# Performance work log

Hardware: AMD Instinct MI355X
Metric: run time of the kernel (lower is better)

The kernel has to match this reference:

```python
import jax, jax.numpy as jnp
import numpy as np

S, WD, TD, CE, CH = 512, 300, 100, 20, 20   # seq len, word dim, tag dim, char emb dim, char lstm hidden
H = 512                                      # main LSTM hidden (per direction)
VOC, TVOC, CVOC, LAB, MAXW = 50000, 50, 100, 50, 16


def lstm_scan(x, W_ih, W_hh, b):
    """Unidirectional LSTM over x:[T,D] -> [T,hid]. PyTorch gate order i,f,g,o."""
    hid = W_hh.shape[1]
    def step(carry, xt):
        h, c = carry
        z = xt @ W_ih.T + h @ W_hh.T + b
        i, f, g, o = jnp.split(z, 4)
        c = jax.nn.sigmoid(f) * c + jax.nn.sigmoid(i) * jnp.tanh(g)
        h = jax.nn.sigmoid(o) * jnp.tanh(c)
        return (h, c), h
    h0 = jnp.zeros((hid,), x.dtype)
    _, hs = jax.lax.scan(step, (h0, h0), x)
    return hs


def setup_inputs() -> dict:
    key = jax.random.key(0)
    ks = jax.random.split(key, 40)
    n = lambda i, shape: jax.random.normal(ks[i], shape, jnp.float32) * 0.05
    return {
        "sentence": jax.random.randint(ks[0], (S,), 0, VOC),
        "tags": jax.random.randint(ks[1], (S,), 0, TVOC),
        "chars": jax.random.randint(ks[2], (S, MAXW), 0, CVOC),
        "char_lengths": jnp.maximum(1, jax.random.randint(ks[3], (S,), 0, MAXW + 1)),
        "best_arcs": jax.random.randint(ks[4], (S,), 0, S),
        "word_emb": n(5, (VOC, WD)),
        "tag_emb": n(6, (TVOC, TD)),
        "char_emb": n(7, (CVOC, CE)),
        "att_W": n(8, (1, CE)), "att_b": n(9, (1,)),
        "W_ih_f": n(10, (4 * H, WD + TD)), "W_hh_f": n(11, (4 * H, H)), "b_f": n(12, (4 * H,)),
        "W_ih_b": n(13, (4 * H, WD + TD)), "W_hh_b": n(14, (4 * H, H)), "b_b": n(15, (4 * H,)),
        "cW_ih": n(16, (4 * CH, CE)), "cW_hh": n(17, (4 * CH, CH)), "cb": n(18, (4 * CH,)),
        "arc_dep_W": n(19, (H, 2 * H)), "arc_dep_b": n(20, (H,)),
        "arc_head_W": n(21, (H, 2 * H)), "arc_head_b": n(22, (H,)),
        "label_dep_W": n(23, (H, 2 * H)), "label_dep_b": n(24, (H,)),
        "label_head_W": n(25, (H, 2 * H)), "label_head_b": n(26, (H,)),
        "biaff_arc_W": n(27, (H, H + 1)),
        "biaff_label_W": n(28, (LAB, H + 1, H + 1)),
    }


def reference(sentence, tags, chars, char_lengths, best_arcs,
              word_emb, tag_emb, char_emb, att_W, att_b,
              W_ih_f, W_hh_f, b_f, W_ih_b, W_hh_b, b_b,
              cW_ih, cW_hh, cb,
              arc_dep_W, arc_dep_b, arc_head_W, arc_head_b,
              label_dep_W, label_dep_b, label_head_W, label_head_b,
              biaff_arc_W, biaff_label_W):
    size = sentence.shape[0]
    we = word_emb[sentence]          # [S, WD]
    te = tag_emb[tags]               # [S, TD]

    # --- per-word char LSTM + attention (original python loop, here vmapped over padded words) ---
    ce = char_emb[chars]             # [S, Lmax, CE]
    def per_word(x, L):
        hs = lstm_scan(x, cW_ih, cW_hh, cb)                  # [Lmax, CH]
        hs = hs * (jnp.arange(x.shape[0]) < L)[:, None]      # zero padded steps
        gram = hs.T @ hs                                     # [CH, CH]
        return gram @ att_W.T + att_b                        # [CH, 1]
    char_feats = jax.vmap(per_word)(ce, char_lengths)        # [S, CH, 1]
    char_embeds = char_feats[:, :, 0].T                      # [CH, S] (cat dim=1 in torch)

    # --- main BiLSTM (dropout in eval mode = identity) ---
    embeds = jnp.concatenate([we, te], axis=1)               # [S, WD+TD]
    hf = lstm_scan(embeds, W_ih_f, W_hh_f, b_f)              # [S, H]
    hb = lstm_scan(embeds[::-1], W_ih_b, W_hh_b, b_b)[::-1]  # [S, H]
    lstm_out = jnp.concatenate([hf, hb], axis=1)             # [S, 2H]

    mlp = lambda W, b: jax.nn.relu(lstm_out @ W.T + b)       # MLP(2H -> H)
    arc_dep = mlp(arc_dep_W, arc_dep_b)
    arc_head = mlp(arc_head_W, arc_head_b)
    label_dep = mlp(label_dep_W, label_dep_b)
    label_head = mlp(label_head_W, label_head_b)

    ones = jnp.ones((size, 1), lstm_out.dtype)
    arc_head_a = jnp.concatenate([arc_head, ones], axis=1)     # [S, H+1]
    label_dep_a = jnp.concatenate([label_dep, ones], axis=1)   # [S, H+1]
    label_head_a = jnp.concatenate([label_head, ones], axis=1) # [S, H+1]

    arc_scores = jax.nn.softmax((arc_head_a @ biaff_arc_W.T) @ arc_dep.T, axis=1)  # [S, S]

    # label_head @ W_l @ label_dep^T for every label l -> [LAB, S, S]
    ls = jnp.einsum('sh,lhk,tk->lst', label_head_a, biaff_label_W, label_dep_a)
    sel = ls[:, best_arcs, jnp.arange(size)]                   # [LAB, S]
    label_scores = jax.nn.log_softmax(sel, axis=0)

    return (arc_scores, label_scores, char_embeds)
```

## Files before the change

kernel.cpp:

```cpp
#include <hip/hip_runtime.h>
#include <hip/hip_fp16.h>


static __device__ __forceinline__ float sigm(float x) { return 1.f / (1.f + __expf(-x)); }
static __device__ __forceinline__ float ftanh(float x) {
    x = fminf(15.f, fmaxf(-15.f, x));
    float e = __expf(2.f * x);
    return (e - 1.f) / (e + 1.f);
}

typedef _Float16 h2_t __attribute__((ext_vector_type(2)));
typedef _Float16 h8_t __attribute__((ext_vector_type(8)));
typedef float f4_t __attribute__((ext_vector_type(4)));
union U32H2 { unsigned u; h2_t h; unsigned short s[2]; };

static __device__ __forceinline__ float dot2f(unsigned wa, unsigned hb, float c) {
#if __has_builtin(__builtin_amdgcn_fdot2)
    U32H2 a, b; a.u = wa; b.u = hb;
    return __builtin_amdgcn_fdot2(a.h, b.h, c, false);
#else
    U32H2 a, b; a.u = wa; b.u = hb;
    return c + (float)a.h[0] * (float)b.h[0] + (float)a.h[1] * (float)b.h[1];
#endif
}
static __device__ __forceinline__ unsigned short f2h16(float x) {
    return __half_as_ushort(__float2half(x));
}

__global__ void gather_k(const int* __restrict__ sentence, const int* __restrict__ tags,
                         const float* __restrict__ word_emb, const float* __restrict__ tag_emb,
                         float* __restrict__ embeds) {
    int t = blockIdx.x;
    int w = sentence[t], tg = tags[t];
    for (int j = threadIdx.x; j < 400; j += blockDim.x) {
        float v = (j < 300) ? word_emb[w * 300 + j] : tag_emb[tg * 100 + (j - 300)];
        embeds[t * 400 + j] = v;
    }
}

static __device__ __forceinline__ void gemm_body(
    const float* __restrict__ A, int lda, const float* __restrict__ B, int ldb,
    const float* __restrict__ bias, int bias_stride,
    float* __restrict__ C, int ldc, int M, int K, int revA, int doRelu) {
    __shared__ float As[16][65];
    __shared__ float Bs[16][65];
    int tx = threadIdx.x & 15, ty = threadIdx.x >> 4;
    int bm = blockIdx.y * 64, bn = blockIdx.x * 64;
    float acc[4][4] = {};
    for (int k0 = 0; k0 < K; k0 += 16) {
#pragma unroll
        for (int i = 0; i < 4; ++i) {
            int e = threadIdx.x + i * 256;
            int m = e >> 4, kk = e & 15;
            int row = bm + m; if (revA) row = M - 1 - row;
            As[kk][m] = A[(size_t)row * lda + k0 + kk];
            Bs[kk][m] = B[(size_t)(bn + m) * ldb + k0 + kk];
        }
        __syncthreads();
#pragma unroll
        for (int kk = 0; kk < 16; ++kk) {
            float a0 = As[kk][ty * 4 + 0], a1 = As[kk][ty * 4 + 1];
            float a2 = As[kk][ty * 4 + 2], a3 = As[kk][ty * 4 + 3];
            float b0 = Bs[kk][tx * 4 + 0], b1 = Bs[kk][tx * 4 + 1];
            float b2 = Bs[kk][tx * 4 + 2], b3 = Bs[kk][tx * 4 + 3];
            acc[0][0] += a0 * b0; acc[0][1] += a0 * b1; acc[0][2] += a0 * b2; acc[0][3] += a0 * b3;
            acc[1][0] += a1 * b0; acc[1][1] += a1 * b1; acc[1][2] += a1 * b2; acc[1][3] += a1 * b3;
            acc[2][0] += a2 * b0; acc[2][1] += a2 * b1; acc[2][2] += a2 * b2; acc[2][3] += a2 * b3;
            acc[3][0] += a3 * b0; acc[3][1] += a3 * b1; acc[3][2] += a3 * b2; acc[3][3] += a3 * b3;
        }
        __syncthreads();
    }
#pragma unroll
    for (int i = 0; i < 4; ++i) {
#pragma unroll
        for (int j = 0; j < 4; ++j) {
            int n = bn + tx * 4 + j;
            float v = acc[i][j];
            if (bias) v += bias[(size_t)n * bias_stride];
            if (doRelu) v = fmaxf(v, 0.f);
            C[(size_t)(bm + ty * 4 + i) * ldc + n] = v;
        }
    }
}

__global__ __launch_bounds__(256) void gemm_abT(
    const float* __restrict__ A, int lda, const float* __restrict__ B, int ldb,
    const float* __restrict__ bias, int bias_stride,
    float* __restrict__ C, int ldc, int M, int N, int K, int revA, int doRelu) {
    gemm_body(A, lda, B, ldb, bias, bias_stride, C, ldc, M, K, revA, doRelu);
}

__global__ __launch_bounds__(256) void gemm_heads(
    const float* __restrict__ A,
    const float* W0, const float* B0, float* C0,
    const float* W1, const float* B1, float* C1,
    const float* W2, const float* B2, float* C2,
    const float* W3, const float* B3, float* C3) {
    const float* W; const float* bias; float* C;
    switch (blockIdx.z) {
        case 0: W = W0; bias = B0; C = C0; break;
        case 1: W = W1; bias = B1; C = C1; break;
        case 2: W = W2; bias = B2; C = C2; break;
        default: W = W3; bias = B3; C = C3; break;
    }
    gemm_body(A, 1024, W, 1024, bias, 1, C, 512, 512, 1024, 0, 1);
}

__global__ __launch_bounds__(256) void gemm_xproj(
    const float* __restrict__ A,
    const float* Wf, const float* bf, float* Cf,
    const float* Wb, const float* bb, float* Cb) {
    const float* W = blockIdx.z ? Wb : Wf;
    const float* bias = blockIdx.z ? bb : bf;
    float* C = blockIdx.z ? Cb : Cf;
    gemm_body(A, 400, W, 400, bias, 1, C, 2048, 512, 400, blockIdx.z, 0);
}

__global__ __launch_bounds__(256) void lstm_rec(
    const float* __restrict__ W_hh_f, const float* __restrict__ W_hh_b,
    const float* __restrict__ xpf, const float* __restrict__ xpb,
    float* __restrict__ lstm_out, unsigned long long* hq) {
    int wg = blockIdx.x;
    int dir = wg >> 4, s = wg & 15;
    int tid = threadIdx.x;
    int wv = tid >> 6;
    int lane = tid & 63;
    int g = tid & 31, p = tid >> 5;
    const float* Whh = dir ? W_hh_b : W_hh_f;
    const float* xp = dir ? xpb : xpf;

    __shared__ float red[2][1024];

    unsigned Wreg[4][32];
#pragma unroll
    for (int q = 0; q < 4; ++q) {
        int gr = q * 512 + s * 32 + g;
        const float* wrow = Whh + (size_t)gr * 512 + p * 64;
#pragma unroll
        for (int u = 0; u < 32; ++u) {
            unsigned lo = f2h16(wrow[2 * u]);
            unsigned hi = f2h16(wrow[2 * u + 1]);
            Wreg[q][u] = lo | (hi << 16);
        }
    }

    float c = 0.f;
    unsigned long long* hbase = hq + dir * 512;
    int qidx = wv * 64 + lane;

    for (int t = 0; t < 512; ++t) {
        float x0 = 0.f, x1 = 0.f, x2 = 0.f, x3 = 0.f;
        if (tid < 32) {
            const float* x = xp + (size_t)t * 2048;
            int col = s * 32 + tid;
            x0 = x[col]; x1 = x[512 + col]; x2 = x[1024 + col]; x3 = x[1536 + col];
        }

        unsigned long long* hin = hbase + (t & 1) * 256;
        unsigned tag = (unsigned)t & 0xffffu;
        unsigned long long v = __hip_atomic_load(hin + qidx, __ATOMIC_RELAXED,
                                                 __HIP_MEMORY_SCOPE_AGENT);
        while ((((unsigned)(v >> 16)) & 0xffffu) != tag || ((unsigned)(v >> 48)) != tag)
            v = __hip_atomic_load(hin + qidx, __ATOMIC_RELAXED, __HIP_MEMORY_SCOPE_AGENT);
        unsigned hw = (unsigned)(v & 0xffffu) | (((unsigned)((v >> 32) & 0xffffu)) << 16);

        float a0 = 0.f, a1 = 0.f, a2 = 0.f, a3 = 0.f;
        int half_base = lane & 32;
#pragma unroll
        for (int u = 0; u < 32; ++u) {
            unsigned hwu = (unsigned)__shfl((int)hw, half_base + u);
            a0 = dot2f(Wreg[0][u], hwu, a0);
            a1 = dot2f(Wreg[1][u], hwu, a1);
            a2 = dot2f(Wreg[2][u], hwu, a2);
            a3 = dot2f(Wreg[3][u], hwu, a3);
        }
        float* r = &red[t & 1][p * 128 + g * 4];
        r[0] = a0; r[1] = a1; r[2] = a2; r[3] = a3;
        __syncthreads();

        if (tid < 32) {
            float z0 = 0.f, z1 = 0.f, z2 = 0.f, z3 = 0.f;
            const float* rb = red[t & 1];
#pragma unroll
            for (int pp = 0; pp < 8; ++pp) {
                const float* rr = rb + pp * 128 + tid * 4;
                z0 += rr[0]; z1 += rr[1]; z2 += rr[2]; z3 += rr[3];
            }
            z0 += x0; z1 += x1; z2 += x2; z3 += x3;
            c = sigm(z1) * c + sigm(z0) * ftanh(z2);
            float hn = sigm(z3) * ftanh(c);
            int col = s * 32 + tid;
            int row = dir ? (511 - t) : t;
            lstm_out[(size_t)row * 1024 + dir * 512 + col] = hn;

            unsigned tw = (unsigned)f2h16(hn) | (((unsigned)(t + 1) & 0xffffu) << 16);
            unsigned other = (unsigned)__shfl_down((int)tw, 1);
            if ((tid & 1) == 0) {
                unsigned long long qv = (unsigned long long)tw |
                                        ((unsigned long long)other << 32);
                __hip_atomic_store(hbase + ((t + 1) & 1) * 256 + (col >> 1), qv,
                                   __ATOMIC_RELAXED, __HIP_MEMORY_SCOPE_AGENT);
            }
        }
    }
}

__global__ __launch_bounds__(64) void char_k(
    const int* __restrict__ chars, const int* __restrict__ char_lengths,
    const float* __restrict__ char_emb, const float* __restrict__ att_W,
    const float* __restrict__ att_b, const float* __restrict__ cW_ih,
    const float* __restrict__ cW_hh, const float* __restrict__ cb,
    float* __restrict__ out2) {
    int w = blockIdx.x, tid = threadIdx.x;
    __shared__ float Wih[1600], Whh[1600], cbs[80], attsh[20];
    __shared__ float xsh[20], hsh[20], prodsh[20];
    for (int i = tid; i < 1600; i += 64) { Wih[i] = cW_ih[i]; Whh[i] = cW_hh[i]; }
    for (int i = tid; i < 80; i += 64) cbs[i] = cb[i];
    if (tid < 20) { attsh[tid] = att_W[tid]; hsh[tid] = 0.f; }
    __syncthreads();

    int L = char_lengths[w];
    float c = 0.f, accj = 0.f;
    for (int t = 0; t < 16; ++t) {
        if (tid < 20) xsh[tid] = char_emb[(size_t)chars[w * 16 + t] * 20 + tid];
        __syncthreads();
        float hn = 0.f;
        if (tid < 20) {
            float z[4];
#pragma unroll
            for (int q = 0; q < 4; ++q) {
                int r = q * 20 + tid;
                float sacc = cbs[r];
                for (int d = 0; d < 20; ++d)
                    sacc += Wih[r * 20 + d] * xsh[d] + Whh[r * 20 + d] * hsh[d];
                z[q] = sacc;
            }
            c = sigm(z[1]) * c + sigm(z[0]) * ftanh(z[2]);
            hn = sigm(z[3]) * ftanh(c);
        }
        __syncthreads();
        if (tid < 20) { hsh[tid] = hn; prodsh[tid] = hn * attsh[tid]; }
        __syncthreads();
        if (tid < 20 && t < L) {
            float st = 0.f;
            for (int k = 0; k < 20; ++k) st += prodsh[k];
            accj += hn * st;
        }
        __syncthreads();
    }
    if (tid < 20) out2[tid * 512 + w] = accj + att_b[0];
}

__global__ void uv_k(const int* __restrict__ best_arcs,
                     const float* __restrict__ label_head, const float* __restrict__ label_dep,
                     float* __restrict__ U, float* __restrict__ V) {
    int t = blockIdx.x;
    int ba = best_arcs[t];
    for (int j = threadIdx.x; j < 516; j += blockDim.x) {
        float u = (j < 512) ? label_head[(size_t)ba * 512 + j] : (j == 512 ? 1.f : 0.f);
        float v = (j < 512) ? label_dep[(size_t)t * 512 + j] : (j == 512 ? 1.f : 0.f);
        U[t * 516 + j] = u;
        V[t * 516 + j] = v;
    }
}

__global__ void uconv_k(const float* __restrict__ U, _Float16* __restrict__ Uh) {
    int t = blockIdx.x;
    for (int h = threadIdx.x; h < 544; h += blockDim.x)
        Uh[(size_t)t * 544 + h] = (_Float16)((h < 513) ? U[(size_t)t * 516 + h] : 0.f);
}

__global__ __launch_bounds__(256) void bconv_k(const float* __restrict__ B,
                                               _Float16* __restrict__ Bh) {
    __shared__ _Float16 Ts[64][68];
    int h0 = blockIdx.x * 64, k0 = blockIdx.y * 64, l = blockIdx.z;
    int tid = threadIdx.x;
    const float* Bl = B + (size_t)l * 513 * 513;
    _Float16* BhL = Bh + (size_t)l * 576 * 544;

    int tr = tid >> 4, tc = tid & 15;
#pragma unroll
    for (int i = 0; i < 4; ++i) {
        int hl = tr + i * 16;
        int h = h0 + hl;
#pragma unroll
        for (int j = 0; j < 4; ++j) {
            int k = k0 + tc * 4 + j;
            float v = (h < 513 && k < 513) ? Bl[(size_t)h * 513 + k] : 0.f;
            Ts[hl][tc * 4 + j] = (_Float16)v;
        }
    }
    __syncthreads();

    int cr = tid >> 2;
    int hb = (tid & 3) * 16;
    int hg = h0 + hb;
    if (hg < 544) {
        __align__(16) _Float16 tmp[16];
#pragma unroll
        for (int j = 0; j < 16; ++j) tmp[j] = Ts[hb + j][cr];
        uint4* dst = (uint4*)(BhL + (size_t)(k0 + cr) * 544 + hg);
        dst[0] = ((const uint4*)tmp)[0];
        dst[1] = ((const uint4*)tmp)[1];
    }
}

__global__ __launch_bounds__(256) void label_mfma(
    const _Float16* __restrict__ Uh,
    const _Float16* __restrict__ Bh,
    const float* __restrict__ V,
    float* __restrict__ sel) {
    __shared__ _Float16 Us[64][40];
    __shared__ _Float16 Bs[64][40];
    int l = blockIdx.z;
    int t0 = blockIdx.y * 64, k0 = blockIdx.x * 64;
    int tid = threadIdx.x;
    int w = tid >> 6, lane = tid & 63, m = lane & 15, q = lane >> 4;
    const _Float16* Bl = Bh + (size_t)l * 576 * 544;
    int srow = tid >> 2, scol = (tid & 3) * 8;

    f4_t acc[4];
#pragma unroll
    for (int c = 0; c < 4; ++c) acc[c] = 0;

    for (int h0 = 0; h0 < 544; h0 += 32) {
        uint4 ud = *(const uint4*)(Uh + (size_t)(t0 + srow) * 544 + h0 + scol);
        uint4 bd = *(const uint4*)(Bl + (size_t)(k0 + srow) * 544 + h0 + scol);
        __syncthreads();
        *(uint4*)(&Us[srow][scol]) = ud;
        *(uint4*)(&Bs[srow][scol]) = bd;
        __syncthreads();

        h8_t a  = *(const h8_t*)(&Us[w * 16 + m][q * 8]);
        h8_t b0 = *(const h8_t*)(&Bs[ 0 + m][q * 8]);
        h8_t b1 = *(const h8_t*)(&Bs[16 + m][q * 8]);
        h8_t b2 = *(const h8_t*)(&Bs[32 + m][q * 8]);
        h8_t b3 = *(const h8_t*)(&Bs[48 + m][q * 8]);
        acc[0] = __builtin_amdgcn_mfma_f32_16x16x32_f16(a, b0, acc[0], 0, 0, 0);
        acc[1] = __builtin_amdgcn_mfma_f32_16x16x32_f16(a, b1, acc[1], 0, 0, 0);
        acc[2] = __builtin_amdgcn_mfma_f32_16x16x32_f16(a, b2, acc[2], 0, 0, 0);
        acc[3] = __builtin_amdgcn_mfma_f32_16x16x32_f16(a, b3, acc[3], 0, 0, 0);
    }

    float* selp = sel + (size_t)l * 512;
#pragma unroll
    for (int r = 0; r < 4; ++r) {
        int t = t0 + w * 16 + q * 4 + r;
        float vsum = 0.f;
#pragma unroll
        for (int c = 0; c < 4; ++c) {
            int k = k0 + c * 16 + m;
            float vv = (k < 513) ? V[(size_t)t * 516 + k] : 0.f;
            vsum += acc[c][r] * vv;
        }
#pragma unroll
        for (int off = 1; off < 16; off <<= 1)
            vsum += __shfl_xor(vsum, off);
        if (m == 0) atomicAdd(selp + t, vsum);
    }
}

__global__ __launch_bounds__(256) void label_k(
    const float* __restrict__ U, const float* __restrict__ V,
    const float* __restrict__ BW, float* __restrict__ sel) {
    __shared__ float Us[16][65];
    __shared__ float Bs[16][65];
    __shared__ float selred[64];
    int l = blockIdx.z;
    int t0 = blockIdx.y * 64, k0 = blockIdx.x * 64;
    const float* Bl = BW + (size_t)l * 513 * 513;
    int tx = threadIdx.x & 15, ty = threadIdx.x >> 4;
    float acc[4][4] = {};
    for (int h0 = 0; h0 < 513; h0 += 16) {
#pragma unroll
        for (int i = 0; i < 4; ++i) {
            int e = threadIdx.x + i * 256;
            int a = e >> 4, hh = e & 15;
            int h = h0 + hh;
            Us[hh][a] = (h < 513) ? U[(size_t)(t0 + a) * 516 + h] : 0.f;
            int kc = k0 + a;
            Bs[hh][a] = (h < 513 && kc < 513) ? Bl[(size_t)h * 513 + kc] : 0.f;
        }
        __syncthreads();
#pragma unroll
        for (int hh = 0; hh < 16; ++hh) {
            float a0 = Us[hh][ty * 4 + 0], a1 = Us[hh][ty * 4 + 1];
            float a2 = Us[hh][ty * 4 + 2], a3 = Us[hh][ty * 4 + 3];
            float b0 = Bs[hh][tx * 4 + 0], b1 = Bs[hh][tx * 4 + 1];
            float b2 = Bs[hh][tx * 4 + 2], b3 = Bs[hh][tx * 4 + 3];
            acc[0][0] += a0 * b0; acc[0][1] += a0 * b1; acc[0][2] += a0 * b2; acc[0][3] += a0 * b3;
            acc[1][0] += a1 * b0; acc[1][1] += a1 * b1; acc[1][2] += a1 * b2; acc[1][3] += a1 * b3;
            acc[2][0] += a2 * b0; acc[2][1] += a2 * b1; acc[2][2] += a2 * b2; acc[2][3] += a2 * b3;
            acc[3][0] += a3 * b0; acc[3][1] += a3 * b1; acc[3][2] += a3 * b2; acc[3][3] += a3 * b3;
        }
        __syncthreads();
    }
    if (threadIdx.x < 64) selred[threadIdx.x] = 0.f;
    __syncthreads();
#pragma unroll
    for (int i = 0; i < 4; ++i) {
        int t = t0 + ty * 4 + i;
        float sacc = 0.f;
#pragma unroll
        for (int j = 0; j < 4; ++j) {
            int k = k0 + tx * 4 + j;
            float vv = (k < 513) ? V[(size_t)t * 516 + k] : 0.f;
            sacc += acc[i][j] * vv;
        }
        atomicAdd(&selred[ty * 4 + i], sacc);
    }
    __syncthreads();
    if (threadIdx.x < 64)
        atomicAdd(&sel[(size_t)l * 512 + t0 + threadIdx.x], selred[threadIdx.x]);
}

__global__ __launch_bounds__(256) void softmax_rows(float* __restrict__ Smat) {
    __shared__ float sdata[256];
    int i = blockIdx.x, tid = threadIdx.x;
    float* row = Smat + (size_t)i * 512;
    float m = -1e30f;
    for (int j = tid; j < 512; j += 256) m = fmaxf(m, row[j]);
    sdata[tid] = m; __syncthreads();
    for (int off = 128; off > 0; off >>= 1) {
        if (tid < off) sdata[tid] = fmaxf(sdata[tid], sdata[tid + off]);
        __syncthreads();
    }
    m = sdata[0]; __syncthreads();
    float ssum = 0.f;
    for (int j = tid; j < 512; j += 256) { float e = __expf(row[j] - m); row[j] = e; ssum += e; }
    sdata[tid] = ssum; __syncthreads();
    for (int off = 128; off > 0; off >>= 1) {
        if (tid < off) sdata[tid] += sdata[tid + off];
        __syncthreads();
    }
    float inv = 1.f / sdata[0];
    for (int j = tid; j < 512; j += 256) row[j] *= inv;
}

__global__ void lsm_k(const float* __restrict__ sel, float* __restrict__ out1) {
    int t = blockIdx.x * blockDim.x + threadIdx.x;
    if (t >= 512) return;
    float m = -1e30f;
    for (int l = 0; l < 50; ++l) m = fmaxf(m, sel[l * 512 + t]);
    float ssum = 0.f;
    for (int l = 0; l < 50; ++l) ssum += __expf(sel[l * 512 + t] - m);
    float lse = m + __logf(ssum);
    for (int l = 0; l < 50; ++l) out1[l * 512 + t] = sel[l * 512 + t] - lse;
}

extern "C" void kernel_launch(void* const* d_in, const int* in_sizes, int n_in,
                              void* d_out, int out_size, void* d_ws, size_t ws_size,
                              hipStream_t stream) {
    const int* sentence     = (const int*)d_in[0];
    const int* tags         = (const int*)d_in[1];
    const int* chars        = (const int*)d_in[2];
    const int* char_lengths = (const int*)d_in[3];
    const int* best_arcs    = (const int*)d_in[4];
    const float* word_emb   = (const float*)d_in[5];
    const float* tag_emb    = (const float*)d_in[6];
    const float* char_emb   = (const float*)d_in[7];
    const float* att_W      = (const float*)d_in[8];
    const float* att_b      = (const float*)d_in[9];
    const float* W_ih_f     = (const float*)d_in[10];
    const float* W_hh_f     = (const float*)d_in[11];
    const float* b_f        = (const float*)d_in[12];
    const float* W_ih_b     = (const float*)d_in[13];
    const float* W_hh_b     = (const float*)d_in[14];
    const float* b_b        = (const float*)d_in[15];
    const float* cW_ih      = (const float*)d_in[16];
    const float* cW_hh      = (const float*)d_in[17];
    const float* cb         = (const float*)d_in[18];
    const float* arc_dep_W  = (const float*)d_in[19];
    const float* arc_dep_b  = (const float*)d_in[20];
    const float* arc_head_W = (const float*)d_in[21];
    const float* arc_head_b = (const float*)d_in[22];
    const float* label_dep_W  = (const float*)d_in[23];
    const float* label_dep_b  = (const float*)d_in[24];
    const float* label_head_W = (const float*)d_in[25];
    const float* label_head_b = (const float*)d_in[26];
    const float* biaff_arc_W   = (const float*)d_in[27];
    const float* biaff_label_W = (const float*)d_in[28];

    float* ws = (float*)d_ws;
    float* out = (float*)d_out;

    const size_t o_embeds = 0;
    const size_t o_xf     = 204800;
    const size_t o_xb     = 1253376;
    const size_t o_lstm   = 2301952;
    const size_t o_heads  = 2826240;
    const size_t o_P      = 3874816;
    const size_t o_U      = 4136960;
    const size_t o_V      = 4401152;
    const size_t o_sel    = 4665344;
    const size_t o_hG     = 4690944;
    const size_t o_Uh     = 4692992;
    const size_t o_Bh     = 4832256;
    const size_t ws_need  = (o_Bh + 7833600) * 4;

    const bool use_mfma_label = (ws_size >= ws_need);

    hipMemsetAsync(ws + o_hG, 0, 8192, stream);
    hipMemsetAsync(ws + o_sel, 0, 25600 * sizeof(float), stream);

    gather_k<<<512, 128, 0, stream>>>(sentence, tags, word_emb, tag_emb, ws + o_embeds);
    char_k<<<512, 64, 0, stream>>>(chars, char_lengths, char_emb, att_W, att_b,
                                   cW_ih, cW_hh, cb, out + 287744);

    if (use_mfma_label)
        bconv_k<<<dim3(9, 9, 50), 256, 0, stream>>>(biaff_label_W, (_Float16*)(ws + o_Bh));

    gemm_xproj<<<dim3(32, 8, 2), 256, 0, stream>>>(ws + o_embeds,
                                                   W_ih_f, b_f, ws + o_xf,
                                                   W_ih_b, b_b, ws + o_xb);

    lstm_rec<<<32, 256, 0, stream>>>(W_hh_f, W_hh_b, ws + o_xf, ws + o_xb,
                                     ws + o_lstm, (unsigned long long*)(ws + o_hG));

    gemm_heads<<<dim3(8, 8, 4), 256, 0, stream>>>(ws + o_lstm,
        arc_dep_W,    arc_dep_b,    ws + o_heads + 0,
        arc_head_W,   arc_head_b,   ws + o_heads + 262144,
        label_dep_W,  label_dep_b,  ws + o_heads + 524288,
        label_head_W, label_head_b, ws + o_heads + 786432);

    uv_k<<<512, 128, 0, stream>>>(best_arcs, ws + o_heads + 786432, ws + o_heads + 524288,
                                  ws + o_U, ws + o_V);

    gemm_abT<<<dim3(8, 8), 256, 0, stream>>>(ws + o_heads + 262144, 512, biaff_arc_W, 513,
                                             biaff_arc_W + 512, 513,
                                             ws + o_P, 512, 512, 512, 512, 0, 0);
    gemm_abT<<<dim3(8, 8), 256, 0, stream>>>(ws + o_P, 512, ws + o_heads + 0, 512, nullptr, 0,
                                             out, 512, 512, 512, 512, 0, 0);
    softmax_rows<<<512, 256, 0, stream>>>(out);

    if (use_mfma_label) {
        uconv_k<<<512, 64, 0, stream>>>(ws + o_U, (_Float16*)(ws + o_Uh));
        label_mfma<<<dim3(9, 8, 50), 256, 0, stream>>>(
            (const _Float16*)(ws + o_Uh), (const _Float16*)(ws + o_Bh),
            ws + o_V, ws + o_sel);
    } else {
        label_k<<<dim3(9, 8, 50), 256, 0, stream>>>(ws + o_U, ws + o_V, biaff_label_W,
                                                    ws + o_sel);
    }
    lsm_k<<<2, 256, 0, stream>>>(ws + o_sel, out + 262144);
}
```

Baseline: 1.527 ms.

## Fuse LSTM recurrence with side work and move head MLPs to fp16 MFMA

Merges the LSTM recurrence, biaffine weight conversion, char LSTM and head-weight fp16 conversion into one large kernel. The 32 recurrence blocks then run alongside the independent blocks instead of serialising with them. The recurrence is remapped so each gate column is reduced across 8 lanes with shuffles instead of through shared memory and a syncthreads, and each lane polls four hidden-state words. The head MLPs now use fp16 MFMA on an fp16 LSTM output. Risks include fp16 accuracy loss, the spin-waiting blocks depending on co-residency with thousands of other blocks, and the workspace overlap of o_Wh16 with the embeddings.

Result: slower. 1.967 ms (+28.9%).

```diff
diff --git a/kernel.cpp b/kernel.cpp
--- a/kernel.cpp
+++ b/kernel.cpp
@@ -90,22 +90,6 @@
     gemm_body(A, lda, B, ldb, bias, bias_stride, C, ldc, M, K, revA, doRelu);
 }
 
-__global__ __launch_bounds__(256) void gemm_heads(
-    const float* __restrict__ A,
-    const float* W0, const float* B0, float* C0,
-    const float* W1, const float* B1, float* C1,
-    const float* W2, const float* B2, float* C2,
-    const float* W3, const float* B3, float* C3) {
-    const float* W; const float* bias; float* C;
-    switch (blockIdx.z) {
-        case 0: W = W0; bias = B0; C = C0; break;
-        case 1: W = W1; bias = B1; C = C1; break;
-        case 2: W = W2; bias = B2; C = C2; break;
-        default: W = W3; bias = B3; C = C3; break;
-    }
-    gemm_body(A, 1024, W, 1024, bias, 1, C, 512, 512, 1024, 0, 1);
-}
-
 __global__ __launch_bounds__(256) void gemm_xproj(
     const float* __restrict__ A,
     const float* Wf, const float* bf, float* Cf,
@@ -116,139 +100,256 @@
     gemm_body(A, 400, W, 400, bias, 1, C, 2048, 512, 400, blockIdx.z, 0);
 }
 
-__global__ __launch_bounds__(256) void lstm_rec(
+__global__ __launch_bounds__(256) void fused_k(
     const float* __restrict__ W_hh_f, const float* __restrict__ W_hh_b,
     const float* __restrict__ xpf, const float* __restrict__ xpb,
-    float* __restrict__ lstm_out, unsigned long long* hq) {
-    int wg = blockIdx.x;
-    int dir = wg >> 4, s = wg & 15;
-    int tid = threadIdx.x;
-    int wv = tid >> 6;
-    int lane = tid & 63;
-    int g = tid & 31, p = tid >> 5;
-    const float* Whh = dir ? W_hh_b : W_hh_f;
-    const float* xp = dir ? xpb : xpf;
-
-    __shared__ float red[2][1024];
-
-    unsigned Wreg[4][32];
-#pragma unroll
-    for (int q = 0; q < 4; ++q) {
-        int gr = q * 512 + s * 32 + g;
-        const float* wrow = Whh + (size_t)gr * 512 + p * 64;
-#pragma unroll
-        for (int u = 0; u < 32; ++u) {
-            unsigned lo = f2h16(wrow[2 * u]);
-            unsigned hi = f2h16(wrow[2 * u + 1]);
-            Wreg[q][u] = lo | (hi << 16);
-        }
-    }
-
-    float c = 0.f;
-    unsigned long long* hbase = hq + dir * 512;
-    int qidx = wv * 64 + lane;
-
-    for (int t = 0; t < 512; ++t) {
-        float x0 = 0.f, x1 = 0.f, x2 = 0.f, x3 = 0.f;
-        if (tid < 32) {
-            const float* x = xp + (size_t)t * 2048;
-            int col = s * 32 + tid;
-            x0 = x[col]; x1 = x[512 + col]; x2 = x[1024 + col]; x3 = x[1536 + col];
-        }
-
-        unsigned long long* hin = hbase + (t & 1) * 256;
-        unsigned tag = (unsigned)t & 0xffffu;
-        unsigned long long v = __hip_atomic_load(hin + qidx, __ATOMIC_RELAXED,
-                                                 __HIP_MEMORY_SCOPE_AGENT);
-        while ((((unsigned)(v >> 16)) & 0xffffu) != tag || ((unsigned)(v >> 48)) != tag)
-            v = __hip_atomic_load(hin + qidx, __ATOMIC_RELAXED, __HIP_MEMORY_SCOPE_AGENT);
-        unsigned hw = (unsigned)(v & 0xffffu) | (((unsigned)((v >> 32) & 0xffffu)) << 16);
-
-        float a0 = 0.f, a1 = 0.f, a2 = 0.f, a3 = 0.f;
-        int half_base = lane & 32;
-#pragma unroll
-        for (int u = 0; u < 32; ++u) {
-            unsigned hwu = (unsigned)__shfl((int)hw, half_base + u);
-            a0 = dot2f(Wreg[0][u], hwu, a0);
-            a1 = dot2f(Wreg[1][u], hwu, a1);
-            a2 = dot2f(Wreg[2][u], hwu, a2);
-            a3 = dot2f(Wreg[3][u], hwu, a3);
-        }
-        float* r = &red[t & 1][p * 128 + g * 4];
-        r[0] = a0; r[1] = a1; r[2] = a2; r[3] = a3;
-        __syncthreads();
-
-        if (tid < 32) {
-            float z0 = 0.f, z1 = 0.f, z2 = 0.f, z3 = 0.f;
-            const float* rb = red[t & 1];
-#pragma unroll
-            for (int pp = 0; pp < 8; ++pp) {
-                const float* rr = rb + pp * 128 + tid * 4;
-                z0 += rr[0]; z1 += rr[1]; z2 += rr[2]; z3 += rr[3];
-            }
-            z0 += x0; z1 += x1; z2 += x2; z3 += x3;
-            c = sigm(z1) * c + sigm(z0) * ftanh(z2);
-            float hn = sigm(z3) * ftanh(c);
-            int col = s * 32 + tid;
-            int row = dir ? (511 - t) : t;
-            lstm_out[(size_t)row * 1024 + dir * 512 + col] = hn;
-
-            unsigned tw = (unsigned)f2h16(hn) | (((unsigned)(t + 1) & 0xffffu) << 16);
-            unsigned other = (unsigned)__shfl_down((int)tw, 1);
-            if ((tid & 1) == 0) {
-                unsigned long long qv = (unsigned long long)tw |
-                                        ((unsigned long long)other << 32);
-                __hip_atomic_store(hbase + ((t + 1) & 1) * 256 + (col >> 1), qv,
-                                   __ATOMIC_RELAXED, __HIP_MEMORY_SCOPE_AGENT);
-            }
-        }
-    }
-}
-
-__global__ __launch_bounds__(64) void char_k(
+    _Float16* __restrict__ lstmh, unsigned long long* hq,
+    const float* __restrict__ BW, _Float16* __restrict__ Bh,
     const int* __restrict__ chars, const int* __restrict__ char_lengths,
     const float* __restrict__ char_emb, const float* __restrict__ att_W,
     const float* __restrict__ att_b, const float* __restrict__ cW_ih,
     const float* __restrict__ cW_hh, const float* __restrict__ cb,
-    float* __restrict__ out2) {
-    int w = blockIdx.x, tid = threadIdx.x;
-    __shared__ float Wih[1600], Whh[1600], cbs[80], attsh[20];
-    __shared__ float xsh[20], hsh[20], prodsh[20];
-    for (int i = tid; i < 1600; i += 64) { Wih[i] = cW_ih[i]; Whh[i] = cW_hh[i]; }
-    for (int i = tid; i < 80; i += 64) cbs[i] = cb[i];
-    if (tid < 20) { attsh[tid] = att_W[tid]; hsh[tid] = 0.f; }
-    __syncthreads();
-
-    int L = char_lengths[w];
-    float c = 0.f, accj = 0.f;
-    for (int t = 0; t < 16; ++t) {
-        if (tid < 20) xsh[tid] = char_emb[(size_t)chars[w * 16 + t] * 20 + tid];
-        __syncthreads();
-        float hn = 0.f;
-        if (tid < 20) {
-            float z[4];
-#pragma unroll
-            for (int q = 0; q < 4; ++q) {
-                int r = q * 20 + tid;
-                float sacc = cbs[r];
-                for (int d = 0; d < 20; ++d)
-                    sacc += Wih[r * 20 + d] * xsh[d] + Whh[r * 20 + d] * hsh[d];
-                z[q] = sacc;
+    float* __restrict__ out2,
+    const float* __restrict__ hw0, const float* __restrict__ hw1,
+    const float* __restrict__ hw2, const float* __restrict__ hw3,
+    _Float16* __restrict__ Wh16) {
+    __shared__ __align__(16) unsigned char smem[16384];
+    int bid = blockIdx.x;
+    int tid = threadIdx.x;
+
+    if (bid < 32) {
+        int dir = bid >> 4, s = bid & 15;
+        int w = tid >> 6, l = tid & 63;
+        int r = l & 7;
+        int dloc = w * 8 + (l >> 3);
+        int col = s * 32 + dloc;
+        const float* Whh = dir ? W_hh_b : W_hh_f;
+        const float* xp = dir ? xpb : xpf;
+
+        unsigned Wreg[4][32];
+#pragma unroll
+        for (int gate = 0; gate < 4; ++gate) {
+            const float* wrow = Whh + (size_t)(gate * 512 + col) * 512 + r * 64;
+#pragma unroll
+            for (int u = 0; u < 32; ++u)
+                Wreg[gate][u] = (unsigned)f2h16(wrow[2 * u]) |
+                                ((unsigned)f2h16(wrow[2 * u + 1]) << 16);
+        }
+
+        float c = 0.f;
+        unsigned long long* hbase = hq + dir * 512;
+        int base_j = r * 32 + ((l >> 3) << 2);
+
+        for (int t = 0; t < 512; ++t) {
+            const float* x = xp + (size_t)t * 2048 + col;
+            float x0 = x[0], x1 = x[512], x2 = x[1024], x3 = x[1536];
+
+            unsigned long long* hin = hbase + (t & 1) * 256 + base_j;
+            unsigned tg = (unsigned)t;
+            unsigned long long v0, v1, v2, v3;
+            for (;;) {
+                v0 = __hip_atomic_load(hin + 0, __ATOMIC_RELAXED, __HIP_MEMORY_SCOPE_AGENT);
+                v1 = __hip_atomic_load(hin + 1, __ATOMIC_RELAXED, __HIP_MEMORY_SCOPE_AGENT);
+                v2 = __hip_atomic_load(hin + 2, __ATOMIC_RELAXED, __HIP_MEMORY_SCOPE_AGENT);
+                v3 = __hip_atomic_load(hin + 3, __ATOMIC_RELAXED, __HIP_MEMORY_SCOPE_AGENT);
+                bool ok = ((((unsigned)(v0 >> 16) & 0xffffu) == tg) & (((unsigned)(v0 >> 48)) == tg))
+                        & ((((unsigned)(v1 >> 16) & 0xffffu) == tg) & (((unsigned)(v1 >> 48)) == tg))
+                        & ((((unsigned)(v2 >> 16) & 0xffffu) == tg) & (((unsigned)(v2 >> 48)) == tg))
+                        & ((((unsigned)(v3 >> 16) & 0xffffu) == tg) & (((unsigned)(v3 >> 48)) == tg));
+                if (ok) break;
             }
-            c = sigm(z[1]) * c + sigm(z[0]) * ftanh(z[2]);
-            hn = sigm(z[3]) * ftanh(c);
-        }
-        __syncthreads();
-        if (tid < 20) { hsh[tid] = hn; prodsh[tid] = hn * attsh[tid]; }
-        __syncthreads();
-        if (tid < 20 && t < L) {
-            float st = 0.f;
-            for (int k = 0; k < 20; ++k) st += prodsh[k];
-            accj += hn * st;
-        }
-        __syncthreads();
-    }
-    if (tid < 20) out2[tid * 512 + w] = accj + att_b[0];
+            unsigned H0 = (unsigned)(v0 & 0xffffu) | (((unsigned)(v0 >> 32) & 0xffffu) << 16);
+            unsigned H1 = (unsigned)(v1 & 0xffffu) | (((unsigned)(v1 >> 32) & 0xffffu) << 16);
+            unsigned H2 = (unsigned)(v2 & 0xffffu) | (((unsigned)(v2 >> 32) & 0xffffu) << 16);
+            unsigned H3 = (unsigned)(v3 & 0xffffu) | (((unsigned)(v3 >> 32) & 0xffffu) << 16);
+
+            float a0 = 0.f, a1 = 0.f, a2 = 0.f, a3 = 0.f;
+#pragma unroll
+            for (int u2 = 0; u2 < 8; ++u2) {
+                int src = u2 * 8 + r;
+                unsigned hv;
+                hv = (unsigned)__shfl((int)H0, src);
+                a0 = dot2f(Wreg[0][u2 * 4 + 0], hv, a0);
+                a1 = dot2f(Wreg[1][u2 * 4 + 0], hv, a1);
+                a2 = dot2f(Wreg[2][u2 * 4 + 0], hv, a2);
+                a3 = dot2f(Wreg[3][u2 * 4 + 0], hv, a3);
+                hv = (unsigned)__shfl((int)H1, src);
+                a0 = dot2f(Wreg[0][u2 * 4 + 1], hv, a0);
+                a1 = dot2f(Wreg[1][u2 * 4 + 1], hv, a1);
+                a2 = dot2f(Wreg[2][u2 * 4 + 1], hv, a2);
+                a3 = dot2f(Wreg[3][u2 * 4 + 1], hv, a3);
+                hv = (unsigned)__shfl((int)H2, src);
+                a0 = dot2f(Wreg[0][u2 * 4 + 2], hv, a0);
+                a1 = dot2f(Wreg[1][u2 * 4 + 2], hv, a1);
+                a2 = dot2f(Wreg[2][u2 * 4 + 2], hv, a2);
+                a3 = dot2f(Wreg[3][u2 * 4 + 2], hv, a3);
+                hv = (unsigned)__shfl((int)H3, src);
+                a0 = dot2f(Wreg[0][u2 * 4 + 3], hv, a0);
+                a1 = dot2f(Wreg[1][u2 * 4 + 3], hv, a1);
+                a2 = dot2f(Wreg[2][u2 * 4 + 3], hv, a2);
+                a3 = dot2f(Wreg[3][u2 * 4 + 3], hv, a3);
+            }
+            a0 += __shfl_xor(a0, 1); a0 += __shfl_xor(a0, 2); a0 += __shfl_xor(a0, 4);
+            a1 += __shfl_xor(a1, 1); a1 += __shfl_xor(a1, 2); a1 += __shfl_xor(a1, 4);
+            a2 += __shfl_xor(a2, 1); a2 += __shfl_xor(a2, 2); a2 += __shfl_xor(a2, 4);
+            a3 += __shfl_xor(a3, 1); a3 += __shfl_xor(a3, 2); a3 += __shfl_xor(a3, 4);
+
+            float z0 = a0 + x0, z1 = a1 + x1, z2 = a2 + x2, z3 = a3 + x3;
+            c = sigm(z1) * c + sigm(z0) * ftanh(z2);
+            float hn = sigm(z3) * ftanh(c);
+
+            unsigned tw = (unsigned)f2h16(hn) | ((unsigned)(t + 1) << 16);
+            unsigned other = (unsigned)__shfl_down((int)tw, 8);
+            if (r == 0) {
+                int row = dir ? (511 - t) : t;
+                lstmh[(size_t)row * 1024 + dir * 512 + col] = (_Float16)hn;
+                if (((l >> 3) & 1) == 0) {
+                    unsigned long long qv = (unsigned long long)tw |
+                                            ((unsigned long long)other << 32);
+                    __hip_atomic_store(hbase + ((t + 1) & 1) * 256 + s * 16 + w * 4 + (l >> 4),
+                                       qv, __ATOMIC_RELAXED, __HIP_MEMORY_SCOPE_AGENT);
+                }
+            }
+        }
+    } else if (bid < 32 + 4050) {
+        typedef _Float16 TsRow[68];
+        TsRow* Ts = (TsRow*)smem;
+        int idx = bid - 32;
+        int lb = idx / 81, rem = idx % 81;
+        int h0 = (rem % 9) * 64, k0 = (rem / 9) * 64;
+        const float* Bl = BW + (size_t)lb * 513 * 513;
+        _Float16* BhL = Bh + (size_t)lb * 576 * 544;
+        int tr = tid >> 4, tc = tid & 15;
+#pragma unroll
+        for (int i = 0; i < 4; ++i) {
+            int hl = tr + i * 16;
+            int h = h0 + hl;
+#pragma unroll
+            for (int j = 0; j < 4; ++j) {
+                int k = k0 + tc * 4 + j;
+                float v = (h < 513 && k < 513) ? Bl[(size_t)h * 513 + k] : 0.f;
+                Ts[hl][tc * 4 + j] = (_Float16)v;
+            }
+        }
+        __syncthreads();
+        int cr = tid >> 2, hb = (tid & 3) * 16;
+        int hg = h0 + hb;
+        if (hg < 544) {
+            __align__(16) _Float16 tmp[16];
+#pragma unroll
+            for (int j = 0; j < 16; ++j) tmp[j] = Ts[hb + j][cr];
+            uint4* dst = (uint4*)(BhL + (size_t)(k0 + cr) * 544 + hg);
+            dst[0] = ((const uint4*)tmp)[0];
+            dst[1] = ((const uint4*)tmp)[1];
+        }
+    } else if (bid < 32 + 4050 + 512) {
+        float* Wih = (float*)smem;
+        float* Whh2 = Wih + 1600;
+        float* cbs = Whh2 + 1600;
+        float* attsh = cbs + 80;
+        float* xsh = attsh + 20;
+        float* hsh = xsh + 20;
+        float* prodsh = hsh + 20;
+        int wd = bid - (32 + 4050);
+        for (int i = tid; i < 1600; i += 256) { Wih[i] = cW_ih[i]; Whh2[i] = cW_hh[i]; }
+        for (int i = tid; i < 80; i += 256) cbs[i] = cb[i];
+        if (tid < 20) { attsh[tid] = att_W[tid]; hsh[tid] = 0.f; }
+        __syncthreads();
+
+        int L = char_lengths[wd];
+        float c = 0.f, accj = 0.f;
+        for (int t = 0; t < 16; ++t) {
+            if (tid < 20) xsh[tid] = char_emb[(size_t)chars[wd * 16 + t] * 20 + tid];
+            __syncthreads();
+            float hn = 0.f;
+            if (tid < 20) {
+                float z[4];
+#pragma unroll
+                for (int q = 0; q < 4; ++q) {
+                    int rr = q * 20 + tid;
+                    float sacc = cbs[rr];
+                    for (int d = 0; d < 20; ++d)
+                        sacc += Wih[rr * 20 + d] * xsh[d] + Whh2[rr * 20 + d] * hsh[d];
+                    z[q] = sacc;
+                }
+                c = sigm(z[1]) * c + sigm(z[0]) * ftanh(z[2]);
+                hn = sigm(z[3]) * ftanh(c);
+            }
+            __syncthreads();
+            if (tid < 20) { hsh[tid] = hn; prodsh[tid] = hn * attsh[tid]; }
+            __syncthreads();
+            if (tid < 20 && t < L) {
+                float st = 0.f;
+                for (int k = 0; k < 20; ++k) st += prodsh[k];
+                accj += hn * st;
+            }
+            __syncthreads();
+        }
+        if (tid < 20) out2[tid * 512 + wd] = accj + att_b[0];
+    } else {
+        int hid = bid - (32 + 4050 + 512);
+        size_t e0 = ((size_t)hid * 256 + tid) * 8;
+        int mat = (int)(e0 >> 19);
+        size_t off = e0 & 524287;
+        const float* src = (mat == 0 ? hw0 : mat == 1 ? hw1 : mat == 2 ? hw2 : hw3) + off;
+        float4 f0 = ((const float4*)src)[0];
+        float4 f1 = ((const float4*)src)[1];
+        __align__(16) _Float16 hv[8];
+        hv[0] = (_Float16)f0.x; hv[1] = (_Float16)f0.y;
+        hv[2] = (_Float16)f0.z; hv[3] = (_Float16)f0.w;
+        hv[4] = (_Float16)f1.x; hv[5] = (_Float16)f1.y;
+        hv[6] = (_Float16)f1.z; hv[7] = (_Float16)f1.w;
+        *(uint4*)(Wh16 + e0) = *(const uint4*)hv;
+    }
+}
+
+__global__ __launch_bounds__(256) void heads_mfma(
+    const _Float16* __restrict__ A,
+    const _Float16* __restrict__ Wh,
+    const float* __restrict__ b0, const float* __restrict__ b1,
+    const float* __restrict__ b2, const float* __restrict__ b3,
+    float* __restrict__ Cout) {
+    __shared__ _Float16 As[64][40];
+    __shared__ _Float16 Bs[64][40];
+    int hd = blockIdx.z;
+    int m0 = blockIdx.y * 64, n0 = blockIdx.x * 64;
+    const _Float16* Bp = Wh + (size_t)hd * 512 * 1024;
+    const float* bias = (hd == 0) ? b0 : (hd == 1) ? b1 : (hd == 2) ? b2 : b3;
+    float* C = Cout + (size_t)hd * 262144;
+    int tid = threadIdx.x;
+    int w = tid >> 6, lane = tid & 63, m = lane & 15, q = lane >> 4;
+    int srow = tid >> 2, scol = (tid & 3) * 8;
+
+    f4_t acc[4];
+#pragma unroll
+    for (int cc = 0; cc < 4; ++cc) acc[cc] = 0;
+
+    for (int k0 = 0; k0 < 1024; k0 += 32) {
+        uint4 ad = *(const uint4*)(A + (size_t)(m0 + srow) * 1024 + k0 + scol);
+        uint4 bd = *(const uint4*)(Bp + (size_t)(n0 + srow) * 1024 + k0 + scol);
+        __syncthreads();
+        *(uint4*)(&As[srow][scol]) = ad;
+        *(uint4*)(&Bs[srow][scol]) = bd;
+        __syncthreads();
+        h8_t a  = *(const h8_t*)(&As[w * 16 + m][q * 8]);
+        h8_t bb0 = *(const h8_t*)(&Bs[ 0 + m][q * 8]);
+        h8_t bb1 = *(const h8_t*)(&Bs[16 + m][q * 8]);
+        h8_t bb2 = *(const h8_t*)(&Bs[32 + m][q * 8]);
+        h8_t bb3 = *(const h8_t*)(&Bs[48 + m][q * 8]);
+        acc[0] = __builtin_amdgcn_mfma_f32_16x16x32_f16(a, bb0, acc[0], 0, 0, 0);
+        acc[1] = __builtin_amdgcn_mfma_f32_16x16x32_f16(a, bb1, acc[1], 0, 0, 0);
+        acc[2] = __builtin_amdgcn_mfma_f32_16x16x32_f16(a, bb2, acc[2], 0, 0, 0);
+        acc[3] = __builtin_amdgcn_mfma_f32_16x16x32_f16(a, bb3, acc[3], 0, 0, 0);
+    }
+#pragma unroll
+    for (int r = 0; r < 4; ++r) {
+        int row = m0 + w * 16 + q * 4 + r;
+#pragma unroll
+        for (int cc = 0; cc < 4; ++cc) {
+            int ncol = n0 + cc * 16 + m;
+            C[(size_t)row * 512 + ncol] = fmaxf(acc[cc][r] + bias[ncol], 0.f);
+        }
+    }
 }
 
 __global__ void uv_k(const int* __restrict__ best_arcs,
@@ -268,41 +369,6 @@
     int t = blockIdx.x;
     for (int h = threadIdx.x; h < 544; h += blockDim.x)
         Uh[(size_t)t * 544 + h] = (_Float16)((h < 513) ? U[(size_t)t * 516 + h] : 0.f);
-}
-
-__global__ __launch_bounds__(256) void bconv_k(const float* __restrict__ B,
-                                               _Float16* __restrict__ Bh) {
-    __shared__ _Float16 Ts[64][68];
-    int h0 = blockIdx.x * 64, k0 = blockIdx.y * 64, l = blockIdx.z;
-    int tid = threadIdx.x;
-    const float* Bl = B + (size_t)l * 513 * 513;
-    _Float16* BhL = Bh + (size_t)l * 576 * 544;
-
-    int tr = tid >> 4, tc = tid & 15;
-#pragma unroll
-    for (int i = 0; i < 4; ++i) {
-        int hl = tr + i * 16;
-        int h = h0 + hl;
-#pragma unroll
-        for (int j = 0; j < 4; ++j) {
-            int k = k0 + tc * 4 + j;
-            float v = (h < 513 && k < 513) ? Bl[(size_t)h * 513 + k] : 0.f;
-            Ts[hl][tc * 4 + j] = (_Float16)v;
-        }
-    }
-    __syncthreads();
-
-    int cr = tid >> 2;
-    int hb = (tid & 3) * 16;
-    int hg = h0 + hb;
-    if (hg < 544) {
-        __align__(16) _Float16 tmp[16];
-#pragma unroll
-        for (int j = 0; j < 16; ++j) tmp[j] = Ts[hb + j][cr];
-        uint4* dst = (uint4*)(BhL + (size_t)(k0 + cr) * 544 + hg);
-        dst[0] = ((const uint4*)tmp)[0];
-        dst[1] = ((const uint4*)tmp)[1];
-    }
 }
 
 __global__ __launch_bounds__(256) void label_mfma(
@@ -330,7 +396,6 @@
         *(uint4*)(&Us[srow][scol]) = ud;
         *(uint4*)(&Bs[srow][scol]) = bd;
         __syncthreads();
-
         h8_t a  = *(const h8_t*)(&Us[w * 16 + m][q * 8]);
         h8_t b0 = *(const h8_t*)(&Bs[ 0 + m][q * 8]);
         h8_t b1 = *(const h8_t*)(&Bs[16 + m][q * 8]);
@@ -358,60 +423,6 @@
             vsum += __shfl_xor(vsum, off);
         if (m == 0) atomicAdd(selp + t, vsum);
     }
-}
-
-__global__ __launch_bounds__(256) void label_k(
-    const float* __restrict__ U, const float* __restrict__ V,
-    const float* __restrict__ BW, float* __restrict__ sel) {
-    __shared__ float Us[16][65];
-    __shared__ float Bs[16][65];
-    __shared__ float selred[64];
-    int l = blockIdx.z;
-    int t0 = blockIdx.y * 64, k0 = blockIdx.x * 64;
-    const float* Bl = BW + (size_t)l * 513 * 513;
-    int tx = threadIdx.x & 15, ty = threadIdx.x >> 4;
-    float acc[4][4] = {};
-    for (int h0 = 0; h0 < 513; h0 += 16) {
-#pragma unroll
-        for (int i = 0; i < 4; ++i) {
-            int e = threadIdx.x + i * 256;
-            int a = e >> 4, hh = e & 15;
-            int h = h0 + hh;
-            Us[hh][a] = (h < 513) ? U[(size_t)(t0 + a) * 516 + h] : 0.f;
-            int kc = k0 + a;
-            Bs[hh][a] = (h < 513 && kc < 513) ? Bl[(size_t)h * 513 + kc] : 0.f;
-        }
-        __syncthreads();
-#pragma unroll
-        for (int hh = 0; hh < 16; ++hh) {
-            float a0 = Us[hh][ty * 4 + 0], a1 = Us[hh][ty * 4 + 1];
-            float a2 = Us[hh][ty * 4 + 2], a3 = Us[hh][ty * 4 + 3];
-            float b0 = Bs[hh][tx * 4 + 0], b1 = Bs[hh][tx * 4 + 1];
-            float b2 = Bs[hh][tx * 4 + 2], b3 = Bs[hh][tx * 4 + 3];
-            acc[0][0] += a0 * b0; acc[0][1] += a0 * b1; acc[0][2] += a0 * b2; acc[0][3] += a0 * b3;
-            acc[1][0] += a1 * b0; acc[1][1] += a1 * b1; acc[1][2] += a1 * b2; acc[1][3] += a1 * b3;
-            acc[2][0] += a2 * b0; acc[2][1] += a2 * b1; acc[2][2] += a2 * b2; acc[2][3] += a2 * b3;
-            acc[3][0] += a3 * b0; acc[3][1] += a3 * b1; acc[3][2] += a3 * b2; acc[3][3] += a3 * b3;
-        }
-        __syncthreads();
-    }
-    if (threadIdx.x < 64) selred[threadIdx.x] = 0.f;
-    __syncthreads();
-#pragma unroll
-    for (int i = 0; i < 4; ++i) {
-        int t = t0 + ty * 4 + i;
-        float sacc = 0.f;
-#pragma unroll
-        for (int j = 0; j < 4; ++j) {
-            int k = k0 + tx * 4 + j;
-            float vv = (k < 513) ? V[(size_t)t * 516 + k] : 0.f;
-            sacc += acc[i][j] * vv;
-        }
-        atomicAdd(&selred[ty * 4 + i], sacc);
-    }
-    __syncthreads();
-    if (threadIdx.x < 64)
-        atomicAdd(&sel[(size_t)l * 512 + t0 + threadIdx.x], selred[threadIdx.x]);
 }
 
 __global__ __launch_bounds__(256) void softmax_rows(float* __restrict__ Smat) {
@@ -485,43 +496,40 @@
     float* out = (float*)d_out;
 
     const size_t o_embeds = 0;
-    const size_t o_xf     = 204800;
-    const size_t o_xb     = 1253376;
-    const size_t o_lstm   = 2301952;
-    const size_t o_heads  = 2826240;
-    const size_t o_P      = 3874816;
-    const size_t o_U      = 4136960;
-    const size_t o_V      = 4401152;
-    const size_t o_sel    = 4665344;
-    const size_t o_hG     = 4690944;
-    const size_t o_Uh     = 4692992;
-    const size_t o_Bh     = 4832256;
-    const size_t ws_need  = (o_Bh + 7833600) * 4;
-
-    const bool use_mfma_label = (ws_size >= ws_need);
+    const size_t o_P      = 204800;
+    const size_t o_U      = 466944;
+    const size_t o_V      = 731136;
+    const size_t o_Uh     = 995328;
+    const size_t o_Wh16   = 0;
+    const size_t o_xf     = 1134592;
+    const size_t o_xb     = 2183168;
+    const size_t o_lstmh  = 3231744;
+    const size_t o_heads  = 3493888;
+    const size_t o_sel    = 4542464;
+    const size_t o_hG     = 4568064;
+    const size_t o_Bh     = 4570112;
 
     hipMemsetAsync(ws + o_hG, 0, 8192, stream);
     hipMemsetAsync(ws + o_sel, 0, 25600 * sizeof(float), stream);
 
     gather_k<<<512, 128, 0, stream>>>(sentence, tags, word_emb, tag_emb, ws + o_embeds);
-    char_k<<<512, 64, 0, stream>>>(chars, char_lengths, char_emb, att_W, att_b,
-                                   cW_ih, cW_hh, cb, out + 287744);
-
-    if (use_mfma_label)
-        bconv_k<<<dim3(9, 9, 50), 256, 0, stream>>>(biaff_label_W, (_Float16*)(ws + o_Bh));
 
     gemm_xproj<<<dim3(32, 8, 2), 256, 0, stream>>>(ws + o_embeds,
                                                    W_ih_f, b_f, ws + o_xf,
                                                    W_ih_b, b_b, ws + o_xb);
 
-    lstm_rec<<<32, 256, 0, stream>>>(W_hh_f, W_hh_b, ws + o_xf, ws + o_xb,
-                                     ws + o_lstm, (unsigned long long*)(ws + o_hG));
-
-    gemm_heads<<<dim3(8, 8, 4), 256, 0, stream>>>(ws + o_lstm,
-        arc_dep_W,    arc_dep_b,    ws + o_heads + 0,
-        arc_head_W,   arc_head_b,   ws + o_heads + 262144,
-        label_dep_W,  label_dep_b,  ws + o_heads + 524288,
-        label_head_W, label_head_b, ws + o_heads + 786432);
+    fused_k<<<5618, 256, 0, stream>>>(
+        W_hh_f, W_hh_b, ws + o_xf, ws + o_xb,
+        (_Float16*)(ws + o_lstmh), (unsigned long long*)(ws + o_hG),
+        biaff_label_W, (_Float16*)(ws + o_Bh),
+        chars, char_lengths, char_emb, att_W, att_b, cW_ih, cW_hh, cb,
+        out + 287744,
+        arc_dep_W, arc_head_W, label_dep_W, label_head_W,
+        (_Float16*)(ws + o_Wh16));
+
+    heads_mfma<<<dim3(8, 8, 4), 256, 0, stream>>>(
+        (const _Float16*)(ws + o_lstmh), (const _Float16*)(ws + o_Wh16),
+        arc_dep_b, arc_head_b, label_dep_b, label_head_b, ws + o_heads);
 
     uv_k<<<512, 128, 0, stream>>>(best_arcs, ws + o_heads + 786432, ws + o_heads + 524288,
                                   ws + o_U, ws + o_V);
@@ -533,14 +541,9 @@
                                              out, 512, 512, 512, 512, 0, 0);
     softmax_rows<<<512, 256, 0, stream>>>(out);
 
-    if (use_mfma_label) {
-        uconv_k<<<512, 64, 0, stream>>>(ws + o_U, (_Float16*)(ws + o_Uh));
-        label_mfma<<<dim3(9, 8, 50), 256, 0, stream>>>(
-            (const _Float16*)(ws + o_Uh), (const _Float16*)(ws + o_Bh),
-            ws + o_V, ws + o_sel);
-    } else {
-        label_k<<<dim3(9, 8, 50), 256, 0, stream>>>(ws + o_U, ws + o_V, biaff_label_W,
-                                                    ws + o_sel);
-    }
+    uconv_k<<<512, 64, 0, stream>>>(ws + o_U, (_Float16*)(ws + o_Uh));
+    label_mfma<<<dim3(9, 8, 50), 256, 0, stream>>>(
+        (const _Float16*)(ws + o_Uh), (const _Float16*)(ws + o_Bh),
+        ws + o_V, ws + o_sel);
     lsm_k<<<2, 256, 0, stream>>>(ws + o_sel, out + 262144);
 }
```
